# Kernel optimization log

Measured on AMD Instinct MI355X. Metric: run time of the kernel, lower is better.

The kernel has to match this reference:

```python
import jax, jax.numpy as jnp
import numpy as np

B, S, DM, DC, L, NS = 4, 2048, 2048, 512, 4, 5  # batch, seq, d_model, d_cortical, n_layers, n_settle


def _ln(x, g, b):
    # torch nn.LayerNorm, eps=1e-5
    m = x.mean(-1, keepdims=True)
    v = ((x - m) ** 2).mean(-1, keepdims=True)
    return (x - m) * jax.lax.rsqrt(v + 1e-5) * g + b


def setup_inputs() -> dict:
    key = jax.random.key(0)
    ks = jax.random.split(key, 20)
    f = lambda k, sh: jax.random.normal(k, sh, jnp.float32) * 0.02
    return dict(
        qwen_final_hidden=jax.random.normal(ks[0], (B, S, DM), jnp.float32),
        obs=jax.random.normal(ks[1], (4, B, S, DM), jnp.float32),
        proj_W=f(ks[2], (4, DC, DM)), proj_b=f(ks[3], (4, DC)),
        fuse_W=f(ks[4], (DC, 4 * DC)), fuse_b=f(ks[5], (DC,)),
        up_W=f(ks[6], (L, DC, DC)), up_b=f(ks[7], (L, DC)),
        lateral_W=f(ks[8], (L, DC, DC)), lateral_b=f(ks[9], (L, DC)),
        precision_logit=f(ks[10], (L, DC)),
        ln_g=jnp.ones((L, DC), jnp.float32), ln_b=jnp.zeros((L, DC), jnp.float32),
        down_W=f(ks[11], (L - 1, DC, DC)), down_b=f(ks[12], (L - 1, DC)),
        out1_W=f(ks[13], (DC, DC)), out1_b=f(ks[14], (DC,)),
        out2_W=f(ks[15], (DM, DC)), out2_b=f(ks[16], (DM,)),
    )


def reference(qwen_final_hidden, obs, proj_W, proj_b, fuse_W, fuse_b,
              up_W, up_b, lateral_W, lateral_b, precision_logit,
              ln_g, ln_b, down_W, down_b, out1_W, out1_b, out2_W, out2_b):
    b, s, dm = qwen_final_hidden.shape
    # per-observed-layer input projections, concatenated along features
    proj = jnp.einsum('obsd,ocd->bsoc', obs, proj_W) + proj_b  # (B,S,4,DC)
    cat = proj.reshape(b, s, -1)
    fused = cat @ fuse_W.T + fuse_b                             # (B,S,DC)
    x0 = fused.reshape(b * s, DC)                               # per-token cortical input

    prec = jax.nn.sigmoid(precision_logit)                      # (L,DC)

    # initial bottom-up pass: activations = compress(x)
    acts = []
    x = x0
    for i in range(L):
        x = _ln(x @ up_W[i].T + up_b[i], ln_g[i], ln_b[i])
        acts.append(x)

    # settling iterations
    for _ in range(NS):
        # top-down predictions computed from pre-sweep activations
        preds = [None] * L
        for i in range(L - 1, 0, -1):
            if i < L - 1:  # top layer has no top-down weights
                preds[i - 1] = acts[i] @ down_W[i].T + down_b[i]
        x = x0
        for i in range(L):
            compressed = _ln(x @ up_W[i].T + up_b[i], ln_g[i], ln_b[i])
            target = preds[i] if preds[i] is not None else acts[i]
            werr = (compressed - target) * prec[i]
            lateral = acts[i] @ lateral_W[i].T + lateral_b[i]
            acts[i] = _ln(acts[i] + 0.5 * werr + 0.1 * lateral, ln_g[i], ln_b[i])
            x = acts[i]

    top = acts[-1]
    h = jax.nn.gelu(top @ out1_W.T + out1_b, approximate=False)
    correction = (h @ out2_W.T + out2_b).reshape(b, s, dm)
    return qwen_final_hidden + correction
```

## Files before the change

kernel.cpp:

```cpp
#include <hip/hip_runtime.h>
#include <hip/hip_bf16.h>
#include <math.h>

#define NTOK 8192
#define DMD  2048
#define DCC  512
#define TOKH 4194304

typedef __attribute__((ext_vector_type(8))) short short8;
typedef __attribute__((ext_vector_type(4))) float f32x4;

__device__ inline float bf2f(unsigned short u) {
    union { unsigned int i; float f; } x; x.i = ((unsigned int)u) << 16; return x.f;
}
__device__ inline unsigned short f2bf(float f) {
    union { float f; unsigned int i; } x; x.f = f;
    unsigned int u = x.i;
    return (unsigned short)((u + 0x7fffu + ((u >> 16) & 1u)) >> 16);
}

typedef const __attribute__((address_space(1))) unsigned int* gas1_t;
typedef __attribute__((address_space(3))) unsigned int* las3_t;
__device__ inline void async16(const void* g, void* l) {
    __builtin_amdgcn_global_load_lds(
        (gas1_t)g,
        (las3_t)(unsigned int)(unsigned long long)l, 16, 0, 0);
}

struct CvtArgs { const float* src[6]; };

__global__ __launch_bounds__(256)
void wcvt_kernel(CvtArgs ca, unsigned short* __restrict__ dst)
{
    const int total = 1310720;
    for (int i = blockIdx.x * 256 + threadIdx.x; i < total; i += gridDim.x * 256) {
        const float* sp; int base;
        if      (i <  262144) { sp = ca.src[0]; base = 0;       }
        else if (i <  524288) { sp = ca.src[1]; base = 262144;  }
        else if (i <  786432) { sp = ca.src[2]; base = 524288;  }
        else if (i <  983040) { sp = ca.src[3]; base = 786432;  }
        else if (i < 1048576) { sp = ca.src[4]; base = 983040;  }
        else                  { sp = ca.src[5]; base = 1048576; }
        float4 v = ((const float4*)sp)[i - base];
        ushort4 o;
        o.x = f2bf(v.x); o.y = f2bf(v.y); o.z = f2bf(v.z); o.w = f2bf(v.w);
        ((ushort4*)dst)[i] = o;
    }
}

__global__ __launch_bounds__(256)
void ptr_kernel(const float* __restrict__ src, unsigned short* __restrict__ dst)
{
    __shared__ float t[32][33];
    const int o  = blockIdx.z;
    const int jb = blockIdx.x * 32;
    const int kb = blockIdx.y * 32;
    const int r  = threadIdx.x >> 3;
    const int c4 = (threadIdx.x & 7) * 4;
    {
        const float* s = src + ((size_t)o * DCC + kb + r) * DMD + jb + c4;
        float4 v = *(const float4*)s;
        t[r][c4+0]=v.x; t[r][c4+1]=v.y; t[r][c4+2]=v.z; t[r][c4+3]=v.w;
    }
    __syncthreads();
    {
        ushort4 u;
        u.x = f2bf(t[c4+0][r]); u.y = f2bf(t[c4+1][r]);
        u.z = f2bf(t[c4+2][r]); u.w = f2bf(t[c4+3][r]);
        *(ushort4*)(dst + ((size_t)o * DMD + jb + r) * DCC + kb + c4) = u;
    }
}

__global__ __launch_bounds__(256)
void bprime_kernel(const float* __restrict__ fuse_W, const float* __restrict__ fuse_b,
                   const float* __restrict__ proj_b, float* __restrict__ bp)
{
    const int row = blockIdx.x * 8 + (threadIdx.x >> 5);
    const int l32 = threadIdx.x & 31;
    const float* r = fuse_W + (size_t)row * (4 * DCC) + l32 * 64;
    const float* p = proj_b + l32 * 64;
    float s = 0.f;
    #pragma unroll
    for (int k = 0; k < 64; k += 4) {
        float4 v = *(const float4*)(r + k);
        float4 q = *(const float4*)(p + k);
        s += v.x*q.x + v.y*q.y + v.z*q.z + v.w*q.w;
    }
    #pragma unroll
    for (int off = 16; off; off >>= 1) s += __shfl_xor(s, off, 64);
    if (l32 == 0) bp[row] = s + fuse_b[row];
}

struct GArgs {
    const unsigned short* A[6];
    const unsigned short* W[6];
    const float*          bias[6];
    const float*          add[6];
    void*                 C[6];
};

template<bool OUTF32, bool GELU>
__global__ __launch_bounds__(256)
void gemm16(GArgs ga, int lda, int ldw, int ldadd, int ldc, int K)
{
    __shared__ unsigned short As[128 * 32];
    __shared__ unsigned short Bs[128 * 32];

    const int z    = blockIdx.z;
    const int tid  = threadIdx.x;
    const int wave = tid >> 6;
    const int lane = tid & 63;

    const int nwg   = gridDim.x * gridDim.y;
    const int bid   = blockIdx.y * gridDim.x + blockIdx.x;
    const int swz   = (bid & 7) * (nwg >> 3) + (bid >> 3);
    const int bn    = (swz % gridDim.x) * 128;
    const int bm    = (swz / gridDim.x) * 128;

    const int wr   = wave >> 1;
    const int wc   = wave & 1;

    const unsigned short* Ap = ga.A[z];
    const unsigned short* Wp = ga.W[z];

    const int lrow = lane >> 2;
    const int lcol = (lane & 3) * 8;

    f32x4 acc[4][4] = {};

    for (int k0 = 0; k0 < K; k0 += 32) {
        #pragma unroll
        for (int r = 0; r < 2; ++r) {
            int c = wave + r * 4;
            async16(Ap + (size_t)(bm + c * 16 + lrow) * lda + k0 + lcol, As + c * 512);
            async16(Wp + (size_t)(bn + c * 16 + lrow) * ldw + k0 + lcol, Bs + c * 512);
        }
        __syncthreads();

        short8 af[4], bfr[4];
        #pragma unroll
        for (int i = 0; i < 4; ++i) {
            af[i]  = *(const short8*)&As[(wr * 64 + i * 16 + (lane & 15)) * 32 + (lane >> 4) * 8];
            bfr[i] = *(const short8*)&Bs[(wc * 64 + i * 16 + (lane & 15)) * 32 + (lane >> 4) * 8];
        }
        #pragma unroll
        for (int mi = 0; mi < 4; ++mi)
            #pragma unroll
            for (int ni = 0; ni < 4; ++ni)
                acc[mi][ni] = __builtin_amdgcn_mfma_f32_16x16x32_bf16(
                    af[mi], bfr[ni], acc[mi][ni], 0, 0, 0);
        __syncthreads();
    }

    const float* bias = ga.bias[z];
    const float* add  = ga.add[z];
    #pragma unroll
    for (int ni = 0; ni < 4; ++ni) {
        int col = bn + wc * 64 + ni * 16 + (lane & 15);
        float bv = bias ? bias[col] : 0.0f;
        #pragma unroll
        for (int mi = 0; mi < 4; ++mi) {
            #pragma unroll
            for (int r = 0; r < 4; ++r) {
                int row = bm + wr * 64 + mi * 16 + (lane >> 4) * 4 + r;
                float vv = acc[mi][ni][r] + bv;
                if (GELU) vv = 0.5f * vv * (1.0f + erff(vv * 0.7071067811865475f));
                if (OUTF32) {
                    if (add) vv += add[(size_t)row * ldadd + col];
                    ((float*)ga.C[z])[(size_t)row * ldc + col] = vv;
                } else {
                    ((unsigned short*)ga.C[z])[(size_t)row * ldc + col] = f2bf(vv);
                }
            }
        }
    }
}

__global__ __launch_bounds__(256)
void x0gemm(const float* __restrict__ obs,
            const unsigned short* __restrict__ M16,
            const float* __restrict__ bp,
            unsigned short* __restrict__ x0)
{
    __shared__ unsigned short As[64 * 32];
    __shared__ unsigned short Bs[128 * 32];

    const int tid  = threadIdx.x;
    const int wave = tid >> 6;
    const int lane = tid & 63;

    const int nwg = gridDim.x * gridDim.y;
    const int bid = blockIdx.y * gridDim.x + blockIdx.x;
    const int swz = (bid & 7) * (nwg >> 3) + (bid >> 3);
    const int bn  = (swz % gridDim.x) * 128;
    const int bm  = (swz / gridDim.x) * 64;

    const int wr = wave >> 1;
    const int wc = wave & 1;
    const int lrow = lane >> 2;
    const int lcol = (lane & 3) * 8;
    const int arow = tid >> 2;
    const int ac8  = (tid & 3) * 8;
    const int l15  = lane & 15;
    const int lh   = lane >> 4;

    f32x4 acc[2][4] = {};

    for (int o = 0; o < 4; ++o) {
        const float* Ap = obs + (size_t)o * NTOK * DMD;
        const unsigned short* Wp = M16 + (size_t)o * DCC * DMD;
        for (int k0 = 0; k0 < DMD; k0 += 32) {
            #pragma unroll
            for (int r = 0; r < 2; ++r) {
                int c = wave + r * 4;
                async16(Wp + (size_t)(bn + c * 16 + lrow) * DMD + k0 + lcol, Bs + c * 512);
            }
            {
                const float* s = Ap + (size_t)(bm + arow) * DMD + k0 + ac8;
                float4 v0 = *(const float4*)(s);
                float4 v1 = *(const float4*)(s + 4);
                short8 o8;
                o8[0]=(short)f2bf(v0.x); o8[1]=(short)f2bf(v0.y);
                o8[2]=(short)f2bf(v0.z); o8[3]=(short)f2bf(v0.w);
                o8[4]=(short)f2bf(v1.x); o8[5]=(short)f2bf(v1.y);
                o8[6]=(short)f2bf(v1.z); o8[7]=(short)f2bf(v1.w);
                *(short8*)&As[arow * 32 + ac8] = o8;
            }
            __syncthreads();

            short8 af[2], bfr[4];
            #pragma unroll
            for (int i = 0; i < 2; ++i)
                af[i] = *(const short8*)&As[(wr * 32 + i * 16 + l15) * 32 + lh * 8];
            #pragma unroll
            for (int i = 0; i < 4; ++i)
                bfr[i] = *(const short8*)&Bs[(wc * 64 + i * 16 + l15) * 32 + lh * 8];
            #pragma unroll
            for (int mi = 0; mi < 2; ++mi)
                #pragma unroll
                for (int ni = 0; ni < 4; ++ni)
                    acc[mi][ni] = __builtin_amdgcn_mfma_f32_16x16x32_bf16(
                        af[mi], bfr[ni], acc[mi][ni], 0, 0, 0);
            __syncthreads();
        }
    }

    #pragma unroll
    for (int ni = 0; ni < 4; ++ni) {
        int col = bn + wc * 64 + ni * 16 + l15;
        float bv = bp[col];
        #pragma unroll
        for (int mi = 0; mi < 2; ++mi)
            #pragma unroll
            for (int r = 0; r < 4; ++r) {
                int row = bm + wr * 32 + mi * 16 + lh * 4 + r;
                x0[(size_t)row * DCC + col] = f2bf(acc[mi][ni][r] + bv);
            }
    }
}

__device__ inline int csw(int rl, int col) {
    int s = ((rl >> 2) & 3) ^ (rl & 3);
    return rl * 512 + (col ^ (s << 4));
}

template<int MODE>
__global__ __launch_bounds__(512)
void gemm_fused(const unsigned short* __restrict__ Ap,
                const unsigned short* __restrict__ Wp,
                const float* __restrict__ bias,
                const float* __restrict__ g,
                const float* __restrict__ b,
                const unsigned short* a_in,
                const unsigned short* t_in,
                const unsigned short* __restrict__ lat_in,
                const float* __restrict__ logit,
                unsigned short* outp)
{
    __shared__ unsigned short Bs[2][512 * 32];
    __shared__ unsigned short As2[2][32 * 32];
    __shared__ float red[2][8][32];

    const int tid  = threadIdx.x;
    const int wave = tid >> 6;
    const int lane = tid & 63;
    const int lrow = lane >> 2;
    const int lc8  = (lane & 3) * 8;
    const int bm   = blockIdx.x * 32;
    const int l15  = lane & 15;
    const int lh   = lane >> 4;

    f32x4 acc[2][4] = {};

    if (wave < 2)
        async16(Ap + (size_t)(bm + wave * 16 + lrow) * DCC + lc8, &As2[0][wave * 512]);
    #pragma unroll
    for (int r = 0; r < 4; ++r)
        async16(Wp + (size_t)((r * 8 + wave) * 16 + lrow) * DCC + lc8,
                &Bs[0][(r * 8 + wave) * 512]);
    __syncthreads();

    for (int t = 0; t < 16; ++t) {
        const int cur = t & 1;
        if (t < 15) {
            const int k0 = (t + 1) * 32;
            if (wave < 2)
                async16(Ap + (size_t)(bm + wave * 16 + lrow) * DCC + k0 + lc8,
                        &As2[cur ^ 1][wave * 512]);
            #pragma unroll
            for (int r = 0; r < 4; ++r)
                async16(Wp + (size_t)((r * 8 + wave) * 16 + lrow) * DCC + k0 + lc8,
                        &Bs[cur ^ 1][(r * 8 + wave) * 512]);
        }
        short8 af[2], bfr[4];
        #pragma unroll
        for (int mi = 0; mi < 2; ++mi)
            af[mi] = *(const short8*)&As2[cur][(mi * 16 + l15) * 32 + lh * 8];
        #pragma unroll
        for (int ni = 0; ni < 4; ++ni)
            bfr[ni] = *(const short8*)&Bs[cur][(wave * 64 + ni * 16 + l15) * 32 + lh * 8];
        #pragma unroll
        for (int mi = 0; mi < 2; ++mi)
            #pragma unroll
            for (int ni = 0; ni < 4; ++ni)
                acc[mi][ni] = __builtin_amdgcn_mfma_f32_16x16x32_bf16(
                    af[mi], bfr[ni], acc[mi][ni], 0, 0, 0);
        __syncthreads();
    }

    float bv[4], gv[4], bbv[4];
    #pragma unroll
    for (int ni = 0; ni < 4; ++ni) {
        int col = wave * 64 + ni * 16 + l15;
        bv[ni] = bias[col]; gv[ni] = g[col]; bbv[ni] = b[col];
    }

    float ps[2][4], pq[2][4];
    #pragma unroll
    for (int mi = 0; mi < 2; ++mi)
        #pragma unroll
        for (int rr = 0; rr < 4; ++rr) {
            float s = 0.f, q = 0.f;
            #pragma unroll
            for (int ni = 0; ni < 4; ++ni) {
                float v = acc[mi][ni][rr] + bv[ni];
                acc[mi][ni][rr] = v;
                s += v; q += v * v;
            }
            #pragma unroll
            for (int off = 1; off < 16; off <<= 1) {
                s += __shfl_xor(s, off, 64);
                q += __shfl_xor(q, off, 64);
            }
            ps[mi][rr] = s; pq[mi][rr] = q;
        }
    if (l15 == 0) {
        #pragma unroll
        for (int mi = 0; mi < 2; ++mi)
            #pragma unroll
            for (int rr = 0; rr < 4; ++rr) {
                int rl = mi * 16 + lh * 4 + rr;
                red[0][wave][rl] = ps[mi][rr];
                red[1][wave][rl] = pq[mi][rr];
            }
    }
    __syncthreads();

    unsigned short* compS = &Bs[0][0];
    #pragma unroll
    for (int mi = 0; mi < 2; ++mi)
        #pragma unroll
        for (int rr = 0; rr < 4; ++rr) {
            int rl = mi * 16 + lh * 4 + rr;
            float s = 0.f, q = 0.f;
            #pragma unroll
            for (int w = 0; w < 8; ++w) { s += red[0][w][rl]; q += red[1][w][rl]; }
            float m1 = s * (1.0f / DCC);
            float r1 = rsqrtf(q * (1.0f / DCC) - m1 * m1 + 1e-5f);
            #pragma unroll
            for (int ni = 0; ni < 4; ++ni) {
                int col = wave * 64 + ni * 16 + l15;
                compS[csw(rl, col)] = f2bf((acc[mi][ni][rr] - m1) * r1 * gv[ni] + bbv[ni]);
            }
        }
    __syncthreads();

    const int c0 = lane * 8;
    if constexpr (MODE == 0) {
        #pragma unroll
        for (int rr = 0; rr < 4; ++rr) {
            const int rl = wave * 4 + rr;
            const size_t gbase = (size_t)(bm + rl) * DCC + c0;
            short8 cm = *(const short8*)&compS[csw(rl, c0)];
            *(short8*)(outp + gbase) = cm;
        }
    } else {
        float gr[8], br[8], pr[8];
        {
            float4 g0 = *(const float4*)(g + c0),     g1 = *(const float4*)(g + c0 + 4);
            float4 b0 = *(const float4*)(b + c0),     b1 = *(const float4*)(b + c0 + 4);
            float4 p0 = *(const float4*)(logit + c0), p1 = *(const float4*)(logit + c0 + 4);
            float gt[8] = {g0.x,g0.y,g0.z,g0.w,g1.x,g1.y,g1.z,g1.w};
            float bt[8] = {b0.x,b0.y,b0.z,b0.w,b1.x,b1.y,b1.z,b1.w};
            float pt[8] = {p0.x,p0.y,p0.z,p0.w,p1.x,p1.y,p1.z,p1.w};
            #pragma unroll
            for (int j = 0; j < 8; ++j) {
                gr[j] = gt[j]; br[j] = bt[j];
                pr[j] = 1.0f / (1.0f + __expf(-pt[j]));
            }
        }
        #pragma unroll
        for (int rr = 0; rr < 4; ++rr) {
            const int rl = wave * 4 + rr;
            const size_t gbase = (size_t)(bm + rl) * DCC + c0;
            short8 cm = *(const short8*)&compS[csw(rl, c0)];
            short8 ar = *(const short8*)(a_in + gbase);
            short8 tr = *(const short8*)(t_in + gbase);
            short8 lr = *(const short8*)(lat_in + gbase);
            float tv[8], s = 0.f, q = 0.f;
            #pragma unroll
            for (int j = 0; j < 8; ++j) {
                float val = bf2f((unsigned short)ar[j])
                          + 0.5f * (bf2f((unsigned short)cm[j]) - bf2f((unsigned short)tr[j])) * pr[j]
                          + 0.1f * bf2f((unsigned short)lr[j]);
                tv[j] = val; s += val; q += val * val;
            }
            #pragma unroll
            for (int off = 1; off < 64; off <<= 1) {
                s += __shfl_xor(s, off, 64);
                q += __shfl_xor(q, off, 64);
            }
            float m2 = s * (1.0f / DCC);
            float r2 = rsqrtf(q * (1.0f / DCC) - m2 * m2 + 1e-5f);
            short8 o;
            #pragma unroll
            for (int j = 0; j < 8; ++j)
                o[j] = (short)f2bf((tv[j] - m2) * r2 * gr[j] + br[j]);
            *(short8*)(outp + gbase) = o;
        }
    }
}

extern "C" void kernel_launch(void* const* d_in, const int* in_sizes, int n_in,
                              void* d_out, int out_size, void* d_ws, size_t ws_size,
                              hipStream_t stream)
{
    const float* qwen   = (const float*)d_in[0];
    const float* obs    = (const float*)d_in[1];
    const float* proj_W = (const float*)d_in[2];
    const float* proj_b = (const float*)d_in[3];
    const float* fuse_W = (const float*)d_in[4];
    const float* fuse_b = (const float*)d_in[5];
    const float* up_W   = (const float*)d_in[6];
    const float* up_b   = (const float*)d_in[7];
    const float* lat_W  = (const float*)d_in[8];
    const float* lat_b  = (const float*)d_in[9];
    const float* plogit = (const float*)d_in[10];
    const float* ln_g   = (const float*)d_in[11];
    const float* ln_b   = (const float*)d_in[12];
    const float* down_W = (const float*)d_in[13];
    const float* down_b = (const float*)d_in[14];
    const float* out1_W = (const float*)d_in[15];
    const float* out1_b = (const float*)d_in[16];
    const float* out2_W = (const float*)d_in[17];
    const float* out2_b = (const float*)d_in[18];
    float* out = (float*)d_out;

    unsigned short* wsu = (unsigned short*)d_ws;
    float*          bp     = (float*)wsu;
    unsigned short* h16    = wsu + 2048;
    unsigned short* x0b    = wsu + 16777216;
    unsigned short* acts16[4] = {
        wsu + 20971520, wsu + 20971520 + TOKH,
        wsu + 20971520 + 2 * TOKH, wsu + 20971520 + 3 * TOKH };
    unsigned short* w16    = wsu + 37748736;
    unsigned short* fuseW16 = w16;
    unsigned short* upW16   = w16 + 1048576;
    unsigned short* latW16  = w16 + 2097152;
    unsigned short* downW16 = w16 + 3145728;
    unsigned short* out1W16 = w16 + 3932160;
    unsigned short* out2W16 = w16 + 4194304;
    unsigned short* projT16 = wsu + 47185920;
    unsigned short* M16     = wsu + 51380224;

    unsigned short* outu = (unsigned short*)d_out;
    unsigned short* pred16a = outu;
    unsigned short* pred16b = outu + TOKH;
    unsigned short* lat16[4] = { outu + 2*TOKH, outu + 3*TOKH, outu + 4*TOKH, outu + 5*TOKH };

    dim3 blk(256);
    dim3 blk512(512);

    {
        CvtArgs ca;
        ca.src[0] = fuse_W; ca.src[1] = up_W;   ca.src[2] = lat_W;
        ca.src[3] = down_W; ca.src[4] = out1_W; ca.src[5] = out2_W;
        wcvt_kernel<<<dim3(2048), blk, 0, stream>>>(ca, w16);
    }
    ptr_kernel<<<dim3(DMD/32, DCC/32, 4), blk, 0, stream>>>(proj_W, projT16);
    bprime_kernel<<<dim3(DCC/8), blk, 0, stream>>>(fuse_W, fuse_b, proj_b, bp);

    {
        GArgs a{};
        for (int o = 0; o < 4; ++o) {
            a.A[o] = fuseW16 + o * DCC;
            a.W[o] = projT16 + (size_t)o * DMD * DCC;
            a.bias[o] = nullptr;
            a.C[o] = M16 + (size_t)o * DCC * DMD;
        }
        gemm16<false, false><<<dim3(DMD/128, DCC/128, 4), blk, 0, stream>>>(
            a, 4 * DCC, DCC, 0, DMD, DCC);
    }

    x0gemm<<<dim3(DCC/128, NTOK/64), blk, 0, stream>>>(obs, M16, bp, x0b);

    dim3 fgrid(NTOK / 32);

    for (int i = 0; i < 4; ++i) {
        gemm_fused<0><<<fgrid, blk512, 0, stream>>>(
            (i == 0) ? x0b : acts16[i - 1],
            upW16 + (size_t)i * DCC * DCC, up_b + i * DCC,
            ln_g + i * DCC, ln_b + i * DCC,
            nullptr, nullptr, nullptr, nullptr, acts16[i]);
    }

    for (int s = 0; s < 5; ++s) {
        {
            GArgs a{};
            a.A[0] = acts16[1]; a.W[0] = downW16 + (size_t)1 * DCC * DCC;
            a.bias[0] = down_b + 1 * DCC; a.C[0] = pred16a;
            a.A[1] = acts16[2]; a.W[1] = downW16 + (size_t)2 * DCC * DCC;
            a.bias[1] = down_b + 2 * DCC; a.C[1] = pred16b;
            for (int i = 0; i < 4; ++i) {
                a.A[2 + i] = acts16[i];
                a.W[2 + i] = latW16 + (size_t)i * DCC * DCC;
                a.bias[2 + i] = lat_b + i * DCC;
                a.C[2 + i] = lat16[i];
            }
            gemm16<false, false><<<dim3(DCC/128, NTOK/128, 6), blk, 0, stream>>>(
                a, DCC, DCC, 0, DCC, DCC);
        }
        for (int i = 0; i < 4; ++i) {
            const unsigned short* tgt =
                (i == 0) ? pred16a : (i == 1) ? pred16b : acts16[i];
            gemm_fused<1><<<fgrid, blk512, 0, stream>>>(
                (i == 0) ? x0b : acts16[i - 1],
                upW16 + (size_t)i * DCC * DCC, up_b + i * DCC,
                ln_g + i * DCC, ln_b + i * DCC,
                acts16[i], tgt, lat16[i], plogit + i * DCC, acts16[i]);
        }
    }

    {
        GArgs a{};
        a.A[0] = acts16[3]; a.W[0] = out1W16; a.bias[0] = out1_b; a.C[0] = h16;
        gemm16<false, true><<<dim3(DCC/128, NTOK/128, 1), blk, 0, stream>>>(
            a, DCC, DCC, 0, DCC, DCC);
    }
    {
        GArgs a{};
        a.A[0] = h16; a.W[0] = out2W16; a.bias[0] = out2_b;
        a.add[0] = qwen; a.C[0] = out;
        gemm16<true, false><<<dim3(DMD/128, NTOK/128, 1), blk, 0, stream>>>(
            a, DCC, DCC, DMD, DMD, DCC);
    }
}
```

Measured before the change: 1.583 ms.

## Double-buffer x0gemm LDS tiles and enlarge M tile to 128 rows

The obs×M GEMM kernel now uses 128x128 output tiles instead of 64x128 and double-buffers both the A and B LDS tiles. The next k-step's fp32 obs loads and async weight loads are issued before the current MFMAs, and the bf16 conversion and store happen after them. This flattens the four observed layers into one 256-step loop and needs only one barrier per step. The aim is to hide global-load latency on this bandwidth-heavy stage and halve weight re-reads, at the cost of more registers and LDS and half as many workgroups.

```diff
diff --git a/kernel.cpp b/kernel.cpp
--- a/kernel.cpp
+++ b/kernel.cpp
@@ -182,8 +182,8 @@
             const float* __restrict__ bp,
             unsigned short* __restrict__ x0)
 {
-    __shared__ unsigned short As[64 * 32];
-    __shared__ unsigned short Bs[128 * 32];
+    __shared__ unsigned short As[2][128 * 32];
+    __shared__ unsigned short Bs[2][128 * 32];
 
     const int tid  = threadIdx.x;
     const int wave = tid >> 6;
@@ -193,56 +193,91 @@
     const int bid = blockIdx.y * gridDim.x + blockIdx.x;
     const int swz = (bid & 7) * (nwg >> 3) + (bid >> 3);
     const int bn  = (swz % gridDim.x) * 128;
-    const int bm  = (swz / gridDim.x) * 64;
+    const int bm  = (swz / gridDim.x) * 128;
 
     const int wr = wave >> 1;
     const int wc = wave & 1;
     const int lrow = lane >> 2;
     const int lcol = (lane & 3) * 8;
-    const int arow = tid >> 2;
-    const int ac8  = (tid & 3) * 8;
     const int l15  = lane & 15;
     const int lh   = lane >> 4;
 
-    f32x4 acc[2][4] = {};
-
-    for (int o = 0; o < 4; ++o) {
-        const float* Ap = obs + (size_t)o * NTOK * DMD;
-        const unsigned short* Wp = M16 + (size_t)o * DCC * DMD;
-        for (int k0 = 0; k0 < DMD; k0 += 32) {
+    const int srow = wave * 32 + (lane >> 2);
+    const int scol = (lane & 3) * 8;
+
+    f32x4 acc[4][4] = {};
+    float4 pa[4];
+
+    {
+        const float* Ap = obs;
+        pa[0] = *(const float4*)(Ap + (size_t)(bm + srow) * DMD + scol);
+        pa[1] = *(const float4*)(Ap + (size_t)(bm + srow) * DMD + scol + 4);
+        pa[2] = *(const float4*)(Ap + (size_t)(bm + srow + 16) * DMD + scol);
+        pa[3] = *(const float4*)(Ap + (size_t)(bm + srow + 16) * DMD + scol + 4);
+        #pragma unroll
+        for (int r = 0; r < 2; ++r) {
+            int c = wave + r * 4;
+            async16(M16 + (size_t)(bn + c * 16 + lrow) * DMD + lcol, &Bs[0][c * 512]);
+        }
+        short8 o8;
+        o8[0]=(short)f2bf(pa[0].x); o8[1]=(short)f2bf(pa[0].y);
+        o8[2]=(short)f2bf(pa[0].z); o8[3]=(short)f2bf(pa[0].w);
+        o8[4]=(short)f2bf(pa[1].x); o8[5]=(short)f2bf(pa[1].y);
+        o8[6]=(short)f2bf(pa[1].z); o8[7]=(short)f2bf(pa[1].w);
+        *(short8*)&As[0][srow * 32 + scol] = o8;
+        o8[0]=(short)f2bf(pa[2].x); o8[1]=(short)f2bf(pa[2].y);
+        o8[2]=(short)f2bf(pa[2].z); o8[3]=(short)f2bf(pa[2].w);
+        o8[4]=(short)f2bf(pa[3].x); o8[5]=(short)f2bf(pa[3].y);
+        o8[6]=(short)f2bf(pa[3].z); o8[7]=(short)f2bf(pa[3].w);
+        *(short8*)&As[0][(srow + 16) * 32 + scol] = o8;
+    }
+    __syncthreads();
+
+    for (int kk = 0; kk < 256; ++kk) {
+        const int cur = kk & 1;
+        if (kk < 255) {
+            const int kk1 = kk + 1;
+            const int o   = kk1 >> 6;
+            const int k0  = (kk1 & 63) << 5;
+            const float* Ap = obs + (size_t)o * NTOK * DMD;
+            pa[0] = *(const float4*)(Ap + (size_t)(bm + srow) * DMD + k0 + scol);
+            pa[1] = *(const float4*)(Ap + (size_t)(bm + srow) * DMD + k0 + scol + 4);
+            pa[2] = *(const float4*)(Ap + (size_t)(bm + srow + 16) * DMD + k0 + scol);
+            pa[3] = *(const float4*)(Ap + (size_t)(bm + srow + 16) * DMD + k0 + scol + 4);
+            const unsigned short* Wp = M16 + (size_t)o * DCC * DMD;
             #pragma unroll
             for (int r = 0; r < 2; ++r) {
                 int c = wave + r * 4;
-                async16(Wp + (size_t)(bn + c * 16 + lrow) * DMD + k0 + lcol, Bs + c * 512);
-            }
-            {
-                const float* s = Ap + (size_t)(bm + arow) * DMD + k0 + ac8;
-                float4 v0 = *(const float4*)(s);
-                float4 v1 = *(const float4*)(s + 4);
-                short8 o8;
-                o8[0]=(short)f2bf(v0.x); o8[1]=(short)f2bf(v0.y);
-                o8[2]=(short)f2bf(v0.z); o8[3]=(short)f2bf(v0.w);
-                o8[4]=(short)f2bf(v1.x); o8[5]=(short)f2bf(v1.y);
-                o8[6]=(short)f2bf(v1.z); o8[7]=(short)f2bf(v1.w);
-                *(short8*)&As[arow * 32 + ac8] = o8;
-            }
-            __syncthreads();
-
-            short8 af[2], bfr[4];
-            #pragma unroll
-            for (int i = 0; i < 2; ++i)
-                af[i] = *(const short8*)&As[(wr * 32 + i * 16 + l15) * 32 + lh * 8];
-            #pragma unroll
-            for (int i = 0; i < 4; ++i)
-                bfr[i] = *(const short8*)&Bs[(wc * 64 + i * 16 + l15) * 32 + lh * 8];
-            #pragma unroll
-            for (int mi = 0; mi < 2; ++mi)
-                #pragma unroll
-                for (int ni = 0; ni < 4; ++ni)
-                    acc[mi][ni] = __builtin_amdgcn_mfma_f32_16x16x32_bf16(
-                        af[mi], bfr[ni], acc[mi][ni], 0, 0, 0);
-            __syncthreads();
-        }
+                async16(Wp + (size_t)(bn + c * 16 + lrow) * DMD + k0 + lcol,
+                        &Bs[cur ^ 1][c * 512]);
+            }
+        }
+        short8 af[4], bfr[4];
+        #pragma unroll
+        for (int i = 0; i < 4; ++i) {
+            af[i]  = *(const short8*)&As[cur][(wr * 64 + i * 16 + l15) * 32 + lh * 8];
+            bfr[i] = *(const short8*)&Bs[cur][(wc * 64 + i * 16 + l15) * 32 + lh * 8];
+        }
+        #pragma unroll
+        for (int mi = 0; mi < 4; ++mi)
+            #pragma unroll
+            for (int ni = 0; ni < 4; ++ni)
+                acc[mi][ni] = __builtin_amdgcn_mfma_f32_16x16x32_bf16(
+                    af[mi], bfr[ni], acc[mi][ni], 0, 0, 0);
+        if (kk < 255) {
+            short8 o8;
+            o8[0]=(short)f2bf(pa[0].x); o8[1]=(short)f2bf(pa[0].y);
+            o8[2]=(short)f2bf(pa[0].z); o8[3]=(short)f2bf(pa[0].w);
+            o8[4]=(short)f2bf(pa[1].x); o8[5]=(short)f2bf(pa[1].y);
+            o8[6]=(short)f2bf(pa[1].z); o8[7]=(short)f2bf(pa[1].w);
+            *(short8*)&As[cur ^ 1][srow * 32 + scol] = o8;
+            o8[0]=(short)f2bf(pa[2].x); o8[1]=(short)f2bf(pa[2].y);
+            o8[2]=(short)f2bf(pa[2].z); o8[3]=(short)f2bf(pa[2].w);
+            o8[4]=(short)f2bf(pa[3].x); o8[5]=(short)f2bf(pa[3].y);
+            o8[6]=(short)f2bf(pa[3].z); o8[7]=(short)f2bf(pa[3].w);
+            *(short8*)&As[cur ^ 1][(srow + 16) * 32 + scol] = o8;
+        }
+        __syncthreads();
     }
 
     #pragma unroll
@@ -250,10 +285,10 @@
         int col = bn + wc * 64 + ni * 16 + l15;
         float bv = bp[col];
         #pragma unroll
-        for (int mi = 0; mi < 2; ++mi)
+        for (int mi = 0; mi < 4; ++mi)
             #pragma unroll
             for (int r = 0; r < 4; ++r) {
-                int row = bm + wr * 32 + mi * 16 + lh * 4 + r;
+                int row = bm + wr * 64 + mi * 16 + lh * 4 + r;
                 x0[(size_t)row * DCC + col] = f2bf(acc[mi][ni][r] + bv);
             }
     }
@@ -512,7 +547,7 @@
             a, 4 * DCC, DCC, 0, DMD, DCC);
     }
 
-    x0gemm<<<dim3(DCC/128, NTOK/64), blk, 0, stream>>>(obs, M16, bp, x0b);
+    x0gemm<<<dim3(DCC/128, NTOK/128), blk, 0, stream>>>(obs, M16, bp, x0b);
 
     dim3 fgrid(NTOK / 32);
 
```

Result: no change. 1.590 ms (+0.5%).

## Replace fused obs GEMM with bf16 pre-convert, batched split-K GEMM and reduction

Applied to the files above, without the earlier changes.

The custom x0gemm kernel, which converted fp32 obs to bf16 inside the GEMM loop and ran all four observed layers serially along K, is removed. In its place, obs is first converted to bf16 in a separate pass. The existing tuned gemm16 kernel then runs the four layers as a batched z-dimension, writing fp32 partials into the output buffer. A small reduction kernel sums the partials, adds the bias and writes bf16 x0. This raises parallelism and reuses the better GEMM path, but adds extra memory traffic for the bf16 obs copy and the fp32 partials.

```diff
diff --git a/kernel.cpp b/kernel.cpp
--- a/kernel.cpp
+++ b/kernel.cpp
@@ -25,6 +25,17 @@
     __builtin_amdgcn_global_load_lds(
         (gas1_t)g,
         (las3_t)(unsigned int)(unsigned long long)l, 16, 0, 0);
+}
+
+__global__ __launch_bounds__(256)
+void cvt_kernel(const float* __restrict__ s, unsigned short* __restrict__ d, int n4)
+{
+    for (int i = blockIdx.x * 256 + threadIdx.x; i < n4; i += gridDim.x * 256) {
+        float4 v = ((const float4*)s)[i];
+        ushort4 o;
+        o.x = f2bf(v.x); o.y = f2bf(v.y); o.z = f2bf(v.z); o.w = f2bf(v.w);
+        ((ushort4*)d)[i] = o;
+    }
 }
 
 struct CvtArgs { const float* src[6]; };
@@ -177,86 +188,22 @@
 }
 
 __global__ __launch_bounds__(256)
-void x0gemm(const float* __restrict__ obs,
-            const unsigned short* __restrict__ M16,
-            const float* __restrict__ bp,
-            unsigned short* __restrict__ x0)
-{
-    __shared__ unsigned short As[64 * 32];
-    __shared__ unsigned short Bs[128 * 32];
-
-    const int tid  = threadIdx.x;
-    const int wave = tid >> 6;
-    const int lane = tid & 63;
-
-    const int nwg = gridDim.x * gridDim.y;
-    const int bid = blockIdx.y * gridDim.x + blockIdx.x;
-    const int swz = (bid & 7) * (nwg >> 3) + (bid >> 3);
-    const int bn  = (swz % gridDim.x) * 128;
-    const int bm  = (swz / gridDim.x) * 64;
-
-    const int wr = wave >> 1;
-    const int wc = wave & 1;
-    const int lrow = lane >> 2;
-    const int lcol = (lane & 3) * 8;
-    const int arow = tid >> 2;
-    const int ac8  = (tid & 3) * 8;
-    const int l15  = lane & 15;
-    const int lh   = lane >> 4;
-
-    f32x4 acc[2][4] = {};
-
-    for (int o = 0; o < 4; ++o) {
-        const float* Ap = obs + (size_t)o * NTOK * DMD;
-        const unsigned short* Wp = M16 + (size_t)o * DCC * DMD;
-        for (int k0 = 0; k0 < DMD; k0 += 32) {
-            #pragma unroll
-            for (int r = 0; r < 2; ++r) {
-                int c = wave + r * 4;
-                async16(Wp + (size_t)(bn + c * 16 + lrow) * DMD + k0 + lcol, Bs + c * 512);
-            }
-            {
-                const float* s = Ap + (size_t)(bm + arow) * DMD + k0 + ac8;
-                float4 v0 = *(const float4*)(s);
-                float4 v1 = *(const float4*)(s + 4);
-                short8 o8;
-                o8[0]=(short)f2bf(v0.x); o8[1]=(short)f2bf(v0.y);
-                o8[2]=(short)f2bf(v0.z); o8[3]=(short)f2bf(v0.w);
-                o8[4]=(short)f2bf(v1.x); o8[5]=(short)f2bf(v1.y);
-                o8[6]=(short)f2bf(v1.z); o8[7]=(short)f2bf(v1.w);
-                *(short8*)&As[arow * 32 + ac8] = o8;
-            }
-            __syncthreads();
-
-            short8 af[2], bfr[4];
-            #pragma unroll
-            for (int i = 0; i < 2; ++i)
-                af[i] = *(const short8*)&As[(wr * 32 + i * 16 + l15) * 32 + lh * 8];
-            #pragma unroll
-            for (int i = 0; i < 4; ++i)
-                bfr[i] = *(const short8*)&Bs[(wc * 64 + i * 16 + l15) * 32 + lh * 8];
-            #pragma unroll
-            for (int mi = 0; mi < 2; ++mi)
-                #pragma unroll
-                for (int ni = 0; ni < 4; ++ni)
-                    acc[mi][ni] = __builtin_amdgcn_mfma_f32_16x16x32_bf16(
-                        af[mi], bfr[ni], acc[mi][ni], 0, 0, 0);
-            __syncthreads();
-        }
-    }
-
-    #pragma unroll
-    for (int ni = 0; ni < 4; ++ni) {
-        int col = bn + wc * 64 + ni * 16 + l15;
-        float bv = bp[col];
-        #pragma unroll
-        for (int mi = 0; mi < 2; ++mi)
-            #pragma unroll
-            for (int r = 0; r < 4; ++r) {
-                int row = bm + wr * 32 + mi * 16 + lh * 4 + r;
-                x0[(size_t)row * DCC + col] = f2bf(acc[mi][ni][r] + bv);
-            }
-    }
+void x0red(const float* __restrict__ partial, const float* __restrict__ bp,
+           unsigned short* __restrict__ x0)
+{
+    const int i = blockIdx.x * 256 + threadIdx.x;
+    float4 a = ((const float4*)partial)[i];
+    float4 b = ((const float4*)(partial + TOKH))[i];
+    float4 c = ((const float4*)(partial + 2 * (size_t)TOKH))[i];
+    float4 d = ((const float4*)(partial + 3 * (size_t)TOKH))[i];
+    const int col = (i * 4) & (DCC - 1);
+    float4 bv = *(const float4*)(bp + col);
+    ushort4 o;
+    o.x = f2bf(a.x + b.x + c.x + d.x + bv.x);
+    o.y = f2bf(a.y + b.y + c.y + d.y + bv.y);
+    o.z = f2bf(a.z + b.z + c.z + d.z + bv.z);
+    o.w = f2bf(a.w + b.w + c.w + d.w + bv.w);
+    ((ushort4*)x0)[i] = o;
 }
 
 __device__ inline int csw(int rl, int col) {
@@ -469,6 +416,7 @@
     unsigned short* wsu = (unsigned short*)d_ws;
     float*          bp     = (float*)wsu;
     unsigned short* h16    = wsu + 2048;
+    unsigned short* M16    = wsu + 8388608;
     unsigned short* x0b    = wsu + 16777216;
     unsigned short* acts16[4] = {
         wsu + 20971520, wsu + 20971520 + TOKH,
@@ -481,8 +429,9 @@
     unsigned short* out1W16 = w16 + 3932160;
     unsigned short* out2W16 = w16 + 4194304;
     unsigned short* projT16 = wsu + 47185920;
-    unsigned short* M16     = wsu + 51380224;
-
+    unsigned short* obs16   = wsu + 47185920;
+
+    float*          part32  = (float*)d_out;
     unsigned short* outu = (unsigned short*)d_out;
     unsigned short* pred16a = outu;
     unsigned short* pred16b = outu + TOKH;
@@ -512,7 +461,21 @@
             a, 4 * DCC, DCC, 0, DMD, DCC);
     }
 
-    x0gemm<<<dim3(DCC/128, NTOK/64), blk, 0, stream>>>(obs, M16, bp, x0b);
+    cvt_kernel<<<dim3(4096), blk, 0, stream>>>(obs, obs16, 16777216);
+
+    {
+        GArgs a{};
+        for (int o = 0; o < 4; ++o) {
+            a.A[o] = obs16 + (size_t)o * NTOK * DMD;
+            a.W[o] = M16 + (size_t)o * DCC * DMD;
+            a.bias[o] = nullptr;
+            a.add[o]  = nullptr;
+            a.C[o] = part32 + (size_t)o * TOKH;
+        }
+        gemm16<true, false><<<dim3(DCC/128, NTOK/128, 4), blk, 0, stream>>>(
+            a, DMD, DMD, 0, DCC, DMD);
+    }
+    x0red<<<dim3(TOKH/4/256), blk, 0, stream>>>(part32, bp, x0b);
 
     dim3 fgrid(NTOK / 32);
 
```

After: 1.552 ms. No clear change (-1.9%).
